# Kernel optimization log

Hardware: AMD Instinct MI355X
Metric: run time of the kernel (lower is better)

Reference implementation:

```python
import jax, jax.numpy as jnp
import numpy as np

P = 4  # polynomial kernel degree


def setup_inputs() -> dict:
    key = jax.random.key(0)
    k1, k2, k3, k4 = jax.random.split(key, 4)
    m, n, d = 16384, 8192, 64
    x_p = jax.random.normal(k1, (m, d), dtype=jnp.float32)
    X = jax.random.normal(k2, (n, d), dtype=jnp.float32)
    alpha = jax.random.uniform(k3, (n,), dtype=jnp.float32, minval=0.0, maxval=0.2)
    b = jax.random.uniform(k4, (1,), dtype=jnp.float32, minval=0.0, maxval=0.2)
    return {"x_p": x_p, "X": X, "alpha": alpha, "b": b}


def reference(x_p, X, alpha, b):
    # SVR prediction with polynomial kernel, vectorized:
    # f(x_p) = sum_i alpha_i * (1 + x_p . X_i)^P + b
    # x_p: [m, d], X: [n, d] -> K: [m, n]
    K = (1.0 + jnp.einsum('md,nd->mn', x_p, X)) ** P
    return K @ alpha + b  # [m]
```

## Files before the change

### kernel.cpp

```cpp
#include <hip/hip_runtime.h>
#include <hip/hip_bf16.h>
#include <stdint.h>


typedef __attribute__((ext_vector_type(8))) short bf16x8;
typedef __attribute__((ext_vector_type(8))) unsigned short ushort8;
typedef __attribute__((ext_vector_type(4))) float f32x4;

#define MM 16384
#define NN 8192
#define DD 64
#define NSPLIT 16
#define CHUNK 64
#define CHUNKS_PER_BLK 8
#define BM 128

__device__ __forceinline__ unsigned short f2bf(float f) {
    uint32_t u = __float_as_uint(f);
    uint32_t r = (u + 0x7FFFu + ((u >> 16) & 1u)) >> 16;
    return (unsigned short)r;
}

__device__ __forceinline__ void gll16(const void* g, void* l) {
    __builtin_amdgcn_global_load_lds(
        (const __attribute__((address_space(1))) unsigned int*)g,
        (__attribute__((address_space(3))) unsigned int*)l, 16, 0, 0);
}

__global__ void convert_kernel(const float* __restrict__ xp,
                               const float* __restrict__ X,
                               const float* __restrict__ alpha,
                               unsigned short* __restrict__ xbf,
                               unsigned short* __restrict__ Xs,
                               float* __restrict__ alpha4f) {
    const int xp4 = MM * DD / 4;
    const int xu = NN * DD / 8;
    const int tot = xp4 + xu;
    int tid0 = blockIdx.x * blockDim.x + threadIdx.x;
    if (tid0 < NN) alpha4f[tid0] = sqrtf(sqrtf(alpha[tid0]));
    int stride = gridDim.x * blockDim.x;
    for (int i = tid0; i < tot; i += stride) {
        if (i < xp4) {
            float4 v = ((const float4*)xp)[i];
            ushort4 o;
            o.x = f2bf(v.x); o.y = f2bf(v.y); o.z = f2bf(v.z); o.w = f2bf(v.w);
            *(ushort4*)(xbf + (size_t)i * 4) = o;
        } else {
            int u = i - xp4;
            int n = u >> 3;
            int slot = u & 7;
            float a4 = sqrtf(sqrtf(alpha[n]));
            float4 va = ((const float4*)X)[n * 16 + slot * 2];
            float4 vb = ((const float4*)X)[n * 16 + slot * 2 + 1];
            ushort8 o;
            o[0] = f2bf(va.x * a4); o[1] = f2bf(va.y * a4);
            o[2] = f2bf(va.z * a4); o[3] = f2bf(va.w * a4);
            o[4] = f2bf(vb.x * a4); o[5] = f2bf(vb.y * a4);
            o[6] = f2bf(vb.z * a4); o[7] = f2bf(vb.w * a4);
            size_t dst = (size_t)(n >> 6) * 4096 + (n & 63) * 64
                       + ((slot ^ (n & 7)) * 8);
            *(ushort8*)(Xs + dst) = o;
        }
    }
}

__global__ __launch_bounds__(256) void svr_main(
        const unsigned short* __restrict__ xbf,
        const unsigned short* __restrict__ Xs,
        const float* __restrict__ alpha4f,
        float* __restrict__ partials) {
    __shared__ char smem[16384];
    const int tid  = threadIdx.x;
    const int lane = tid & 63;
    const int w    = tid >> 6;
    const int r    = lane & 15;
    const int g    = lane >> 4;
    const int mgroup = blockIdx.x >> 4;
    const int ns     = blockIdx.x & 15;

    bf16x8 a[2][2];
#pragma unroll
    for (int mt = 0; mt < 2; ++mt)
#pragma unroll
        for (int ks = 0; ks < 2; ++ks)
            a[mt][ks] = *(const bf16x8*)(
                xbf + (size_t)(mgroup * BM + w * 32 + mt * 16 + r) * DD
                    + ks * 32 + g * 8);

    f32x4 red[2];
#pragma unroll
    for (int mt = 0; mt < 2; ++mt) red[mt] = (f32x4){0.f, 0.f, 0.f, 0.f};

    const int chunk0 = ns * CHUNKS_PER_BLK;

    {
        const char* gs = (const char*)Xs + (size_t)chunk0 * 8192 + tid * 16;
        char* lb = smem + w * 1024;
        gll16(gs, lb);
        gll16(gs + 4096, lb + 4096);
    }
    __syncthreads();

    int cur = 0;
#pragma unroll 1
    for (int c = 0; c < CHUNKS_PER_BLK; ++c) {
        if (c + 1 < CHUNKS_PER_BLK) {
            const char* gs = (const char*)Xs
                           + (size_t)(chunk0 + c + 1) * 8192 + tid * 16;
            char* lb = smem + (cur ^ 1) * 8192 + w * 1024;
            gll16(gs, lb);
            gll16(gs + 4096, lb + 4096);
        }
        const int n0 = (chunk0 + c) * CHUNK;
        float av4[4];
#pragma unroll
        for (int nt = 0; nt < 4; ++nt)
            av4[nt] = alpha4f[n0 + nt * 16 + r];
        bf16x8 b[4][2];
#pragma unroll
        for (int nt = 0; nt < 4; ++nt) {
            const int rr = nt * 16 + r;
            const char* rowp = smem + cur * 8192 + rr * 128;
#pragma unroll
            for (int bh = 0; bh < 2; ++bh) {
                const int slot = (bh * 4 + g) ^ (rr & 7);
                b[nt][bh] = *(const bf16x8*)(rowp + slot * 16);
            }
        }
        f32x4 acc[2][4];
#pragma unroll
        for (int mt = 0; mt < 2; ++mt)
#pragma unroll
            for (int nt = 0; nt < 4; ++nt)
                acc[mt][nt] = (f32x4){av4[nt], av4[nt], av4[nt], av4[nt]};
#pragma unroll
        for (int bh = 0; bh < 2; ++bh)
#pragma unroll
            for (int nt = 0; nt < 4; ++nt)
#pragma unroll
                for (int mt = 0; mt < 2; ++mt)
                    acc[mt][nt] = __builtin_amdgcn_mfma_f32_16x16x32_bf16(
                        a[mt][bh], b[nt][bh], acc[mt][nt], 0, 0, 0);
#pragma unroll
        for (int mt = 0; mt < 2; ++mt)
#pragma unroll
            for (int nt = 0; nt < 4; ++nt)
#pragma unroll
                for (int i = 0; i < 4; ++i) {
                    float t = acc[mt][nt][i];
                    float t2 = t * t;
                    red[mt][i] = fmaf(t2, t2, red[mt][i]);
                }
        __syncthreads();
        cur ^= 1;
    }

#pragma unroll
    for (int mt = 0; mt < 2; ++mt)
#pragma unroll
        for (int i = 0; i < 4; ++i) {
            float v = red[mt][i];
            v += __shfl_xor(v, 1);
            v += __shfl_xor(v, 2);
            v += __shfl_xor(v, 4);
            v += __shfl_xor(v, 8);
            red[mt][i] = v;
        }
    if (r == 0) {
#pragma unroll
        for (int mt = 0; mt < 2; ++mt)
#pragma unroll
            for (int i = 0; i < 4; ++i) {
                int row = mgroup * BM + w * 32 + mt * 16 + g * 4 + i;
                partials[(size_t)ns * MM + row] = red[mt][i];
            }
    }
}

__global__ void finalize_kernel(const float* __restrict__ partials,
                                const float* __restrict__ bbias,
                                float* __restrict__ out) {
    int m = blockIdx.x * blockDim.x + threadIdx.x;
    if (m < MM) {
        float s = bbias[0];
#pragma unroll
        for (int c = 0; c < NSPLIT; ++c) s += partials[(size_t)c * MM + m];
        out[m] = s;
    }
}

extern "C" void kernel_launch(void* const* d_in, const int* in_sizes, int n_in,
                              void* d_out, int out_size, void* d_ws, size_t ws_size,
                              hipStream_t stream) {
    const float* xp    = (const float*)d_in[0];
    const float* X     = (const float*)d_in[1];
    const float* alpha = (const float*)d_in[2];
    const float* b     = (const float*)d_in[3];
    float* out = (float*)d_out;

    unsigned short* xbf = (unsigned short*)d_ws;
    unsigned short* Xs  = xbf + (size_t)MM * DD;
    float* alpha4f = (float*)(Xs + (size_t)NN * DD);
    float* partials = alpha4f + NN;

    hipLaunchKernelGGL(convert_kernel, dim3(1280), dim3(256), 0, stream,
                       xp, X, alpha, xbf, Xs, alpha4f);

    hipLaunchKernelGGL(svr_main, dim3(128 * NSPLIT), dim3(256), 0, stream,
                       xbf, Xs, alpha4f, partials);

    hipLaunchKernelGGL(finalize_kernel, dim3(MM / 256), dim3(256), 0, stream,
                       partials, b, out);
}
```

Baseline: 36.04 us.

## Fuse x_p conversion into main kernel, remap waves over N, drop finalize via atomics

The main kernel now converts x_p from fp32 to bf16 in registers instead of reading a pre-converted copy, so the convert kernel only handles X and alpha and also writes the bias into the output. Each wave now holds all 128 rows (8 m-tiles) and owns a 16-column slice of the chunk, so it loads one B fragment pair per chunk rather than four, and fetches alpha one chunk ahead. Per-split partials and the finalize kernel are replaced by atomicAdd into the output, removing one launch and the partial-buffer traffic. The trade-off is more registers for A fragments, each x_p row being read from global and converted four times per block, and atomic contention across the 16 splits.

```diff
diff --git a/kernel.cpp b/kernel.cpp
--- a/kernel.cpp
+++ b/kernel.cpp
@@ -14,6 +14,7 @@
 #define CHUNK 64
 #define CHUNKS_PER_BLK 8
 #define BM 128
+#define MT 8
 
 __device__ __forceinline__ unsigned short f2bf(float f) {
     uint32_t u = __float_as_uint(f);
@@ -27,48 +28,35 @@
         (__attribute__((address_space(3))) unsigned int*)l, 16, 0, 0);
 }
 
-__global__ void convert_kernel(const float* __restrict__ xp,
-                               const float* __restrict__ X,
+__global__ void convert_kernel(const float* __restrict__ X,
                                const float* __restrict__ alpha,
-                               unsigned short* __restrict__ xbf,
+                               const float* __restrict__ bbias,
                                unsigned short* __restrict__ Xs,
-                               float* __restrict__ alpha4f) {
-    const int xp4 = MM * DD / 4;
-    const int xu = NN * DD / 8;
-    const int tot = xp4 + xu;
+                               float* __restrict__ alpha4f,
+                               float* __restrict__ out) {
     int tid0 = blockIdx.x * blockDim.x + threadIdx.x;
     if (tid0 < NN) alpha4f[tid0] = sqrtf(sqrtf(alpha[tid0]));
-    int stride = gridDim.x * blockDim.x;
-    for (int i = tid0; i < tot; i += stride) {
-        if (i < xp4) {
-            float4 v = ((const float4*)xp)[i];
-            ushort4 o;
-            o.x = f2bf(v.x); o.y = f2bf(v.y); o.z = f2bf(v.z); o.w = f2bf(v.w);
-            *(ushort4*)(xbf + (size_t)i * 4) = o;
-        } else {
-            int u = i - xp4;
-            int n = u >> 3;
-            int slot = u & 7;
-            float a4 = sqrtf(sqrtf(alpha[n]));
-            float4 va = ((const float4*)X)[n * 16 + slot * 2];
-            float4 vb = ((const float4*)X)[n * 16 + slot * 2 + 1];
-            ushort8 o;
-            o[0] = f2bf(va.x * a4); o[1] = f2bf(va.y * a4);
-            o[2] = f2bf(va.z * a4); o[3] = f2bf(va.w * a4);
-            o[4] = f2bf(vb.x * a4); o[5] = f2bf(vb.y * a4);
-            o[6] = f2bf(vb.z * a4); o[7] = f2bf(vb.w * a4);
-            size_t dst = (size_t)(n >> 6) * 4096 + (n & 63) * 64
-                       + ((slot ^ (n & 7)) * 8);
-            *(ushort8*)(Xs + dst) = o;
-        }
-    }
+    if (tid0 < MM) out[tid0] = bbias[0];
+    int n = tid0 >> 3;
+    int slot = tid0 & 7;
+    float a4 = sqrtf(sqrtf(alpha[n]));
+    float4 va = ((const float4*)X)[n * 16 + slot * 2];
+    float4 vb = ((const float4*)X)[n * 16 + slot * 2 + 1];
+    ushort8 o;
+    o[0] = f2bf(va.x * a4); o[1] = f2bf(va.y * a4);
+    o[2] = f2bf(va.z * a4); o[3] = f2bf(va.w * a4);
+    o[4] = f2bf(vb.x * a4); o[5] = f2bf(vb.y * a4);
+    o[6] = f2bf(vb.z * a4); o[7] = f2bf(vb.w * a4);
+    size_t dst = (size_t)(n >> 6) * 4096 + (n & 63) * 64
+               + ((slot ^ (n & 7)) * 8);
+    *(ushort8*)(Xs + dst) = o;
 }
 
 __global__ __launch_bounds__(256) void svr_main(
-        const unsigned short* __restrict__ xbf,
+        const float* __restrict__ xp,
         const unsigned short* __restrict__ Xs,
         const float* __restrict__ alpha4f,
-        float* __restrict__ partials) {
+        float* __restrict__ out) {
     __shared__ char smem[16384];
     const int tid  = threadIdx.x;
     const int lane = tid & 63;
@@ -78,20 +66,29 @@
     const int mgroup = blockIdx.x >> 4;
     const int ns     = blockIdx.x & 15;
 
-    bf16x8 a[2][2];
+    bf16x8 a[MT][2];
 #pragma unroll
-    for (int mt = 0; mt < 2; ++mt)
+    for (int mt = 0; mt < MT; ++mt)
 #pragma unroll
-        for (int ks = 0; ks < 2; ++ks)
-            a[mt][ks] = *(const bf16x8*)(
-                xbf + (size_t)(mgroup * BM + w * 32 + mt * 16 + r) * DD
-                    + ks * 32 + g * 8);
+        for (int ks = 0; ks < 2; ++ks) {
+            const float* p = xp + (size_t)(mgroup * BM + mt * 16 + r) * DD
+                           + ks * 32 + g * 8;
+            float4 v0 = ((const float4*)p)[0];
+            float4 v1 = ((const float4*)p)[1];
+            ushort8 o;
+            o[0] = f2bf(v0.x); o[1] = f2bf(v0.y);
+            o[2] = f2bf(v0.z); o[3] = f2bf(v0.w);
+            o[4] = f2bf(v1.x); o[5] = f2bf(v1.y);
+            o[6] = f2bf(v1.z); o[7] = f2bf(v1.w);
+            a[mt][ks] = __builtin_bit_cast(bf16x8, o);
+        }
 
-    f32x4 red[2];
+    f32x4 red[MT];
 #pragma unroll
-    for (int mt = 0; mt < 2; ++mt) red[mt] = (f32x4){0.f, 0.f, 0.f, 0.f};
+    for (int mt = 0; mt < MT; ++mt) red[mt] = (f32x4){0.f, 0.f, 0.f, 0.f};
 
     const int chunk0 = ns * CHUNKS_PER_BLK;
+    const int rr = w * 16 + r;
 
     {
         const char* gs = (const char*)Xs + (size_t)chunk0 * 8192 + tid * 16;
@@ -99,64 +96,49 @@
         gll16(gs, lb);
         gll16(gs + 4096, lb + 4096);
     }
+    float av_cur = alpha4f[chunk0 * 64 + rr];
     __syncthreads();
 
     int cur = 0;
 #pragma unroll 1
     for (int c = 0; c < CHUNKS_PER_BLK; ++c) {
+        float av_nxt;
         if (c + 1 < CHUNKS_PER_BLK) {
+            av_nxt = alpha4f[(chunk0 + c + 1) * 64 + rr];
             const char* gs = (const char*)Xs
                            + (size_t)(chunk0 + c + 1) * 8192 + tid * 16;
             char* lb = smem + (cur ^ 1) * 8192 + w * 1024;
             gll16(gs, lb);
             gll16(gs + 4096, lb + 4096);
         }
-        const int n0 = (chunk0 + c) * CHUNK;
-        float av4[4];
+        const char* rowp = smem + cur * 8192 + rr * 128;
+        bf16x8 b0 = *(const bf16x8*)(rowp + ((g ^ (rr & 7)) * 16));
+        bf16x8 b1 = *(const bf16x8*)(rowp + (((4 + g) ^ (rr & 7)) * 16));
+        f32x4 acc[MT];
 #pragma unroll
-        for (int nt = 0; nt < 4; ++nt)
-            av4[nt] = alpha4f[n0 + nt * 16 + r];
-        bf16x8 b[4][2];
+        for (int mt = 0; mt < MT; ++mt)
+            acc[mt] = (f32x4){av_cur, av_cur, av_cur, av_cur};
 #pragma unroll
-        for (int nt = 0; nt < 4; ++nt) {
-            const int rr = nt * 16 + r;
-            const char* rowp = smem + cur * 8192 + rr * 128;
+        for (int mt = 0; mt < MT; ++mt)
+            acc[mt] = __builtin_amdgcn_mfma_f32_16x16x32_bf16(a[mt][0], b0, acc[mt], 0, 0, 0);
 #pragma unroll
-            for (int bh = 0; bh < 2; ++bh) {
-                const int slot = (bh * 4 + g) ^ (rr & 7);
-                b[nt][bh] = *(const bf16x8*)(rowp + slot * 16);
+        for (int mt = 0; mt < MT; ++mt)
+            acc[mt] = __builtin_amdgcn_mfma_f32_16x16x32_bf16(a[mt][1], b1, acc[mt], 0, 0, 0);
+#pragma unroll
+        for (int mt = 0; mt < MT; ++mt)
+#pragma unroll
+            for (int i = 0; i < 4; ++i) {
+                float t = acc[mt][i];
+                float t2 = t * t;
+                red[mt][i] = fmaf(t2, t2, red[mt][i]);
             }
-        }
-        f32x4 acc[2][4];
-#pragma unroll
-        for (int mt = 0; mt < 2; ++mt)
-#pragma unroll
-            for (int nt = 0; nt < 4; ++nt)
-                acc[mt][nt] = (f32x4){av4[nt], av4[nt], av4[nt], av4[nt]};
-#pragma unroll
-        for (int bh = 0; bh < 2; ++bh)
-#pragma unroll
-            for (int nt = 0; nt < 4; ++nt)
-#pragma unroll
-                for (int mt = 0; mt < 2; ++mt)
-                    acc[mt][nt] = __builtin_amdgcn_mfma_f32_16x16x32_bf16(
-                        a[mt][bh], b[nt][bh], acc[mt][nt], 0, 0, 0);
-#pragma unroll
-        for (int mt = 0; mt < 2; ++mt)
-#pragma unroll
-            for (int nt = 0; nt < 4; ++nt)
-#pragma unroll
-                for (int i = 0; i < 4; ++i) {
-                    float t = acc[mt][nt][i];
-                    float t2 = t * t;
-                    red[mt][i] = fmaf(t2, t2, red[mt][i]);
-                }
         __syncthreads();
         cur ^= 1;
+        if (c + 1 < CHUNKS_PER_BLK) av_cur = av_nxt;
     }
 
 #pragma unroll
-    for (int mt = 0; mt < 2; ++mt)
+    for (int mt = 0; mt < MT; ++mt)
 #pragma unroll
         for (int i = 0; i < 4; ++i) {
             float v = red[mt][i];
@@ -168,24 +150,12 @@
         }
     if (r == 0) {
 #pragma unroll
-        for (int mt = 0; mt < 2; ++mt)
+        for (int mt = 0; mt < MT; ++mt)
 #pragma unroll
             for (int i = 0; i < 4; ++i) {
-                int row = mgroup * BM + w * 32 + mt * 16 + g * 4 + i;
-                partials[(size_t)ns * MM + row] = red[mt][i];
+                int row = mgroup * BM + mt * 16 + g * 4 + i;
+                atomicAdd(out + row, red[mt][i]);
             }
-    }
-}
-
-__global__ void finalize_kernel(const float* __restrict__ partials,
-                                const float* __restrict__ bbias,
-                                float* __restrict__ out) {
-    int m = blockIdx.x * blockDim.x + threadIdx.x;
-    if (m < MM) {
-        float s = bbias[0];
-#pragma unroll
-        for (int c = 0; c < NSPLIT; ++c) s += partials[(size_t)c * MM + m];
-        out[m] = s;
     }
 }
 
@@ -198,17 +168,12 @@
     const float* b     = (const float*)d_in[3];
     float* out = (float*)d_out;
 
-    unsigned short* xbf = (unsigned short*)d_ws;
-    unsigned short* Xs  = xbf + (size_t)MM * DD;
+    unsigned short* Xs = (unsigned short*)d_ws;
     float* alpha4f = (float*)(Xs + (size_t)NN * DD);
-    float* partials = alpha4f + NN;
 
-    hipLaunchKernelGGL(convert_kernel, dim3(1280), dim3(256), 0, stream,
-                       xp, X, alpha, xbf, Xs, alpha4f);
+    hipLaunchKernelGGL(convert_kernel, dim3(256), dim3(256), 0, stream,
+                       X, alpha, b, Xs, alpha4f, out);
 
     hipLaunchKernelGGL(svr_main, dim3(128 * NSPLIT), dim3(256), 0, stream,
-                       xbf, Xs, alpha4f, partials);
-
-    hipLaunchKernelGGL(finalize_kernel, dim3(MM / 256), dim3(256), 0, stream,
-                       partials, b, out);
+                       xp, Xs, alpha4f, out);
 }
```

New measurement: 85.98 us. 139% more time.

## Software-pipeline MFMA and epilogue across chunks, reduce N-split to four

Applied to the files above, without the earlier changes.

The main loop now uses two accumulator sets, even and odd, so each chunk's pow-4 reduction epilogue runs while the next chunk's MFMAs issue. The alpha loads for the next chunk are prefetched one iteration ahead. NSPLIT drops from 16 to 4 with 32 chunks per block, so the grid shrinks to 512 blocks and the finalize kernel reads fewer partials. The cost is higher register pressure from the doubled accumulators and fewer blocks to fill the GPU.

```diff
diff --git a/kernel.cpp b/kernel.cpp
--- a/kernel.cpp
+++ b/kernel.cpp
@@ -10,9 +10,9 @@
 #define MM 16384
 #define NN 8192
 #define DD 64
-#define NSPLIT 16
+#define NSPLIT 4
 #define CHUNK 64
-#define CHUNKS_PER_BLK 8
+#define CHUNKS_PER_BLK 32
 #define BM 128
 
 __device__ __forceinline__ unsigned short f2bf(float f) {
@@ -64,6 +64,59 @@
     }
 }
 
+#define LOAD_B(bvar, bufp)                                            \
+    {                                                                 \
+        _Pragma("unroll")                                             \
+        for (int nt = 0; nt < 4; ++nt) {                              \
+            const int rr2 = nt * 16 + r;                              \
+            const char* rowp = (bufp) + rr2 * 128;                    \
+            _Pragma("unroll")                                         \
+            for (int bh = 0; bh < 2; ++bh) {                          \
+                const int slot = (bh * 4 + g) ^ (rr2 & 7);            \
+                bvar[nt][bh] = *(const bf16x8*)(rowp + slot * 16);    \
+            }                                                         \
+        }                                                             \
+    }
+
+#define MFMA_SET(accv, bvar, avv)                                     \
+    {                                                                 \
+        _Pragma("unroll")                                             \
+        for (int mt = 0; mt < 2; ++mt)                                \
+            _Pragma("unroll")                                         \
+            for (int nt = 0; nt < 4; ++nt)                            \
+                accv[mt][nt] = (f32x4){avv[nt], avv[nt], avv[nt], avv[nt]}; \
+        _Pragma("unroll")                                             \
+        for (int bh = 0; bh < 2; ++bh)                                \
+            _Pragma("unroll")                                         \
+            for (int nt = 0; nt < 4; ++nt)                            \
+                _Pragma("unroll")                                     \
+                for (int mt = 0; mt < 2; ++mt)                        \
+                    accv[mt][nt] = __builtin_amdgcn_mfma_f32_16x16x32_bf16( \
+                        a[mt][bh], bvar[nt][bh], accv[mt][nt], 0, 0, 0);    \
+    }
+
+#define EPILOGUE(accv)                                                \
+    {                                                                 \
+        _Pragma("unroll")                                             \
+        for (int mt = 0; mt < 2; ++mt)                                \
+            _Pragma("unroll")                                         \
+            for (int nt = 0; nt < 4; ++nt)                            \
+                _Pragma("unroll")                                     \
+                for (int i = 0; i < 4; ++i) {                         \
+                    float t = accv[mt][nt][i];                        \
+                    float t2 = t * t;                                 \
+                    red[mt][i] = fmaf(t2, t2, red[mt][i]);            \
+                }                                                     \
+    }
+
+#define STAGE(cidx)                                                   \
+    {                                                                 \
+        const char* gs = (const char*)Xs + (size_t)(cidx) * 8192 + tid * 16; \
+        char* lb = smem + (cur ^ 1) * 8192 + w * 1024;                \
+        gll16(gs, lb);                                                \
+        gll16(gs + 4096, lb + 4096);                                  \
+    }
+
 __global__ __launch_bounds__(256) void svr_main(
         const unsigned short* __restrict__ xbf,
         const unsigned short* __restrict__ Xs,
@@ -75,8 +128,8 @@
     const int w    = tid >> 6;
     const int r    = lane & 15;
     const int g    = lane >> 4;
-    const int mgroup = blockIdx.x >> 4;
-    const int ns     = blockIdx.x & 15;
+    const int mgroup = blockIdx.x >> 2;
+    const int ns     = blockIdx.x & 3;
 
     bf16x8 a[2][2];
 #pragma unroll
@@ -92,6 +145,7 @@
     for (int mt = 0; mt < 2; ++mt) red[mt] = (f32x4){0.f, 0.f, 0.f, 0.f};
 
     const int chunk0 = ns * CHUNKS_PER_BLK;
+    int cur = 0;
 
     {
         const char* gs = (const char*)Xs + (size_t)chunk0 * 8192 + tid * 16;
@@ -99,61 +153,56 @@
         gll16(gs, lb);
         gll16(gs + 4096, lb + 4096);
     }
+    float av_c[4], av_n[4];
+#pragma unroll
+    for (int nt = 0; nt < 4; ++nt)
+        av_c[nt] = alpha4f[chunk0 * CHUNK + nt * 16 + r];
     __syncthreads();
 
-    int cur = 0;
+    f32x4 accE[2][4], accO[2][4];
+
 #pragma unroll 1
-    for (int c = 0; c < CHUNKS_PER_BLK; ++c) {
-        if (c + 1 < CHUNKS_PER_BLK) {
-            const char* gs = (const char*)Xs
-                           + (size_t)(chunk0 + c + 1) * 8192 + tid * 16;
-            char* lb = smem + (cur ^ 1) * 8192 + w * 1024;
-            gll16(gs, lb);
-            gll16(gs + 4096, lb + 4096);
-        }
-        const int n0 = (chunk0 + c) * CHUNK;
-        float av4[4];
-#pragma unroll
-        for (int nt = 0; nt < 4; ++nt)
-            av4[nt] = alpha4f[n0 + nt * 16 + r];
-        bf16x8 b[4][2];
-#pragma unroll
-        for (int nt = 0; nt < 4; ++nt) {
-            const int rr = nt * 16 + r;
-            const char* rowp = smem + cur * 8192 + rr * 128;
-#pragma unroll
-            for (int bh = 0; bh < 2; ++bh) {
-                const int slot = (bh * 4 + g) ^ (rr & 7);
-                b[nt][bh] = *(const bf16x8*)(rowp + slot * 16);
-            }
-        }
-        f32x4 acc[2][4];
-#pragma unroll
-        for (int mt = 0; mt < 2; ++mt)
+    for (int p = 0; p < CHUNKS_PER_BLK / 2; ++p) {
+        {
+            const int cnext = chunk0 + 2 * p + 1;
+            STAGE(cnext);
 #pragma unroll
             for (int nt = 0; nt < 4; ++nt)
-                acc[mt][nt] = (f32x4){av4[nt], av4[nt], av4[nt], av4[nt]};
-#pragma unroll
-        for (int bh = 0; bh < 2; ++bh)
-#pragma unroll
-            for (int nt = 0; nt < 4; ++nt)
-#pragma unroll
-                for (int mt = 0; mt < 2; ++mt)
-                    acc[mt][nt] = __builtin_amdgcn_mfma_f32_16x16x32_bf16(
-                        a[mt][bh], b[nt][bh], acc[mt][nt], 0, 0, 0);
-#pragma unroll
-        for (int mt = 0; mt < 2; ++mt)
-#pragma unroll
-            for (int nt = 0; nt < 4; ++nt)
-#pragma unroll
-                for (int i = 0; i < 4; ++i) {
-                    float t = acc[mt][nt][i];
-                    float t2 = t * t;
-                    red[mt][i] = fmaf(t2, t2, red[mt][i]);
-                }
+                av_n[nt] = alpha4f[cnext * CHUNK + nt * 16 + r];
+        }
+        {
+            bf16x8 b[4][2];
+            LOAD_B(b, smem + cur * 8192);
+            MFMA_SET(accE, b, av_c);
+        }
+        if (p) EPILOGUE(accO);
         __syncthreads();
         cur ^= 1;
-    }
+#pragma unroll
+        for (int nt = 0; nt < 4; ++nt) av_c[nt] = av_n[nt];
+
+        const int c1 = 2 * p + 1;
+        if (c1 + 1 < CHUNKS_PER_BLK) {
+            const int cnext = chunk0 + c1 + 1;
+            STAGE(cnext);
+#pragma unroll
+            for (int nt = 0; nt < 4; ++nt)
+                av_n[nt] = alpha4f[cnext * CHUNK + nt * 16 + r];
+        }
+        {
+            bf16x8 b[4][2];
+            LOAD_B(b, smem + cur * 8192);
+            MFMA_SET(accO, b, av_c);
+        }
+        EPILOGUE(accE);
+        __syncthreads();
+        cur ^= 1;
+        if (c1 + 1 < CHUNKS_PER_BLK) {
+#pragma unroll
+            for (int nt = 0; nt < 4; ++nt) av_c[nt] = av_n[nt];
+        }
+    }
+    EPILOGUE(accO);
 
 #pragma unroll
     for (int mt = 0; mt < 2; ++mt)
```

Result: faster. 33.98 us (-5.7%).
